# Kernel optimization log

Measured on AMD Instinct MI355X. Metric: run time of the kernel, lower is better.

## Reference

```python
import jax, jax.numpy as jnp
import numpy as np

H = 2048
V = 32000
B = 4            # 2 chosen + 2 rejected sequences
T = 1024
BETA = 0.1
IGNORE_INDEX = -100


def setup_inputs() -> dict:
    key = jax.random.key(0)
    k1, k2, k3, k4, k5 = jax.random.split(key, 5)
    x = jax.random.normal(k1, (B, T, H), dtype=jnp.float32)
    ref_x = jax.random.normal(k2, (B, T, H), dtype=jnp.float32)
    y = jax.random.randint(k3, (B, T), 0, V, dtype=jnp.int64)
    # Linear weights scaled ~1/sqrt(H) so logits are well-conditioned
    W = jax.random.normal(k4, (V, H), dtype=jnp.float32) * (1.0 / np.sqrt(H))
    W_ref = jax.random.normal(k5, (V, H), dtype=jnp.float32) * (1.0 / np.sqrt(H))
    return {"x": x, "ref_x": ref_x, "y": y, "W": W, "W_ref": W_ref}


def _avg_seq_logps(h, W, y, mask):
    # h: [B,T,H], W: [V,H] -> average per-sequence log-prob of the target tokens
    logits = jnp.einsum("bth,vh->btv", h, W)                 # [B,T,V]
    logps = jax.nn.log_softmax(logits, axis=-1)
    y_safe = jnp.where(mask, y, 0)
    per_tok = jnp.take_along_axis(logps, y_safe[..., None], axis=-1)[..., 0]  # [B,T]
    m = mask.astype(logps.dtype)
    return (per_tok * m).sum(-1) / m.sum(-1)                  # [B]


def reference(x, ref_x, y, W, W_ref):
    mask = y != IGNORE_INDEX
    logps = _avg_seq_logps(x, W, y, mask)
    # reference model path is computed without gradients (torch.no_grad in Liger)
    ref_logps = jax.lax.stop_gradient(_avg_seq_logps(ref_x, W_ref, y, mask))
    half = B // 2
    chosen, rejected = logps[:half], logps[half:]
    ref_chosen, ref_rejected = ref_logps[:half], ref_logps[half:]
    logits_diff = BETA * ((chosen - ref_chosen) - (rejected - ref_rejected))
    loss = -jax.nn.log_sigmoid(logits_diff).sum() / half
    return loss
```

## Files before the change

kernel.cpp:

```cpp
#include <hip/hip_runtime.h>
#include <cstdint>
#include <cstddef>

#define HDIM 2048
#define VOCAB 32000
#define BT 4096
#define NVB 125
#define BETA_F 0.1f
#define SCALE_X 16.0f
#define SCALE_W 64.0f
#define INV_SC (1.0f / (SCALE_X * SCALE_W))

typedef float f32x4 __attribute__((ext_vector_type(4)));
typedef long lx2 __attribute__((ext_vector_type(2)));

__device__ __forceinline__ void async_lds16(const void* g, void* l) {
  __builtin_amdgcn_global_load_lds(
      (__attribute__((address_space(1))) void*)g,
      (__attribute__((address_space(3))) void*)l,
      16, 0, 0);
}

#define BAR() __builtin_amdgcn_s_barrier()
#define LGKM0() do { asm volatile("s_waitcnt lgkmcnt(0)" ::: "memory"); \
                     __builtin_amdgcn_sched_barrier(0); } while (0)
#define VMCNT(n) do { asm volatile("s_waitcnt vmcnt(" #n ")" ::: "memory"); \
                      __builtin_amdgcn_sched_barrier(0); } while (0)

__global__ void cast_fp8_kernel(const float* __restrict__ src,
                                uint4* __restrict__ dst, int n16, float scale) {
  int i = blockIdx.x * blockDim.x + threadIdx.x;
  int stride = gridDim.x * blockDim.x;
  for (; i < n16; i += stride) {
    const float4* s = (const float4*)src + (size_t)i * 4;
    uint4 o;
    {
      float4 a = s[0];
      int r = __builtin_amdgcn_cvt_pk_fp8_f32(a.x * scale, a.y * scale, 0, false);
      o.x = __builtin_amdgcn_cvt_pk_fp8_f32(a.z * scale, a.w * scale, r, true);
    }
    {
      float4 a = s[1];
      int r = __builtin_amdgcn_cvt_pk_fp8_f32(a.x * scale, a.y * scale, 0, false);
      o.y = __builtin_amdgcn_cvt_pk_fp8_f32(a.z * scale, a.w * scale, r, true);
    }
    {
      float4 a = s[2];
      int r = __builtin_amdgcn_cvt_pk_fp8_f32(a.x * scale, a.y * scale, 0, false);
      o.z = __builtin_amdgcn_cvt_pk_fp8_f32(a.z * scale, a.w * scale, r, true);
    }
    {
      float4 a = s[3];
      int r = __builtin_amdgcn_cvt_pk_fp8_f32(a.x * scale, a.y * scale, 0, false);
      o.w = __builtin_amdgcn_cvt_pk_fp8_f32(a.z * scale, a.w * scale, r, true);
    }
    dst[i] = o;
  }
}

__global__ __launch_bounds__(512, 2) void gemm_lse256(
    const unsigned char* __restrict__ Xq,
    const unsigned char* __restrict__ Xrq,
    const unsigned char* __restrict__ Wq,
    const unsigned char* __restrict__ Wrq,
    float2* __restrict__ part) {
  __shared__ __align__(16) char lds[2][2][2][8192];

  const int tid = threadIdx.x;
  const int lane = tid & 63;
  const int w = tid >> 6;
  const int wm = w >> 2;
  const int wn = w & 3;
  const int which = blockIdx.y;

  const int lin = blockIdx.x;
  const int nl = (lin & 7) * 250 + (lin >> 3);
  const int mb = nl & 15;
  const int nb = nl >> 4;

  const unsigned char* A = which ? Xrq : Xq;
  const unsigned char* B = which ? Wrq : Wq;
  float2* pp = part + (size_t)which * BT * NVB;

  const int lanep = lane ^ ((lane & 32) >> 4);
  const int rw = w * 16 + (lanep >> 2);
  const int cw = (lanep & 3) * 16;
  const unsigned char* Ag = A + (size_t)(mb * 256 + rw) * HDIM + cw;
  const unsigned char* Bg = B + (size_t)(nb * 256 + rw) * HDIM + cw;

#define STAGE(opsel, buf, h, T) do {                                          \
    const unsigned char* _g = (opsel) ? Bg : Ag;                              \
    async_lds16(_g + (size_t)(h) * 128 * HDIM + (T) * 64,                     \
                &lds[buf][opsel][h][0] + w * 1024);                           \
  } while (0)

  const int l15 = lane & 15;
  const int kbyte = (lane >> 4) * 16;
#define FRAGP(d0, d1, halfptr, row) do {                                      \
    int _r = (row);                                                           \
    int _L = _r * 64 + kbyte;                                                 \
    lx2 _v = *(const lx2*)((halfptr) + (_L ^ (((_r >> 3) & 1) << 5)));        \
    d0 = _v.x; d1 = _v.y;                                                     \
  } while (0)

  const char* A0h = &lds[0][0][wm][0];
  const char* A1h = &lds[1][0][wm][0];
  const char* B0h = &lds[0][1][wn >> 1][0];
  const char* B1h = &lds[1][1][wn >> 1][0];
  const int brow = (wn & 1) * 64;

  f32x4 acc[8][4] = {};
  long aF[4][2], bF[4][2];

#define READ_A(base, mi0) do {                                                \
    _Pragma("unroll") for (int mi = 0; mi < 4; ++mi)                          \
      FRAGP(aF[mi][0], aF[mi][1], base, ((mi0) + mi) * 16 + l15);             \
  } while (0)
#define READ_B(base) do {                                                     \
    _Pragma("unroll") for (int ni = 0; ni < 4; ++ni)                          \
      FRAGP(bF[ni][0], bF[ni][1], base, brow + ni * 16 + l15);                \
  } while (0)
#define MFMA_Q(MI0, NI0) do {                                                 \
    __builtin_amdgcn_s_setprio(1);                                            \
    _Pragma("unroll") for (int kk = 0; kk < 2; ++kk)                          \
    _Pragma("unroll") for (int mi = 0; mi < 4; ++mi)                          \
    _Pragma("unroll") for (int ni = 0; ni < 2; ++ni)                          \
      acc[(MI0) + mi][(NI0) + ni] = __builtin_amdgcn_mfma_f32_16x16x32_fp8_fp8( \
          aF[mi][kk], bF[(NI0) + ni][kk], acc[(MI0) + mi][(NI0) + ni], 0, 0, 0); \
    __builtin_amdgcn_s_setprio(0);                                            \
  } while (0)

  STAGE(0, 0, 0, 0); STAGE(0, 0, 1, 0); STAGE(1, 0, 0, 0); STAGE(1, 0, 1, 0);
  STAGE(1, 1, 0, 1); STAGE(1, 1, 1, 1); STAGE(0, 1, 0, 1);
  VMCNT(3);
  BAR();

  for (int i = 0; i < 16; ++i) {
    const int t1 = 2 * i + 1;
    const int se = (2 * i + 2 > 30) ? 30 : 2 * i + 2;
    const int so = (2 * i + 3 > 31) ? 31 : 2 * i + 3;

    READ_A(A0h, 0);
    READ_B(B0h);
    STAGE(0, 1, 1, t1);
    BAR(); LGKM0();
    MFMA_Q(0, 0);
    BAR();

    STAGE(1, 0, 0, se);
    BAR(); LGKM0();
    MFMA_Q(0, 2);
    BAR();

    READ_A(A0h, 4);
    STAGE(1, 0, 1, se);
    BAR(); LGKM0();
    MFMA_Q(4, 0);
    BAR();

    STAGE(0, 0, 0, se);
    VMCNT(3);
    BAR();
    MFMA_Q(4, 2);
    BAR();

    READ_A(A1h, 0);
    READ_B(B1h);
    STAGE(0, 0, 1, se);
    BAR(); LGKM0();
    MFMA_Q(0, 0);
    BAR();

    STAGE(1, 1, 0, so);
    BAR(); LGKM0();
    MFMA_Q(0, 2);
    BAR();

    READ_A(A1h, 4);
    STAGE(1, 1, 1, so);
    BAR(); LGKM0();
    MFMA_Q(4, 0);
    BAR();

    STAGE(0, 1, 0, so);
    VMCNT(3);
    BAR();
    MFMA_Q(4, 2);
    BAR();
  }
  VMCNT(0);
  BAR();

  float* red = (float*)&lds[0][0][0][0];
#pragma unroll
  for (int mi = 0; mi < 8; ++mi) {
#pragma unroll
    for (int r = 0; r < 4; ++r) {
      float v0 = acc[mi][0][r] * INV_SC;
      float v1 = acc[mi][1][r] * INV_SC;
      float v2 = acc[mi][2][r] * INV_SC;
      float v3 = acc[mi][3][r] * INV_SC;
      float m = fmaxf(fmaxf(v0, v1), fmaxf(v2, v3));
#pragma unroll
      for (int o = 1; o < 16; o <<= 1) m = fmaxf(m, __shfl_xor(m, o, 64));
      float s = __expf(v0 - m) + __expf(v1 - m) + __expf(v2 - m) + __expf(v3 - m);
#pragma unroll
      for (int o = 1; o < 16; o <<= 1) s += __shfl_xor(s, o, 64);
      if (l15 == 0) {
        int row = wm * 128 + mi * 16 + (lane >> 4) * 4 + r;
        red[wn * 256 + row] = m;
        red[1024 + wn * 256 + row] = s;
      }
    }
  }
  __syncthreads();
  if (tid < 256) {
    float m0 = red[tid], m1 = red[256 + tid], m2 = red[512 + tid], m3 = red[768 + tid];
    float M = fmaxf(fmaxf(m0, m1), fmaxf(m2, m3));
    float S = red[1024 + tid] * __expf(m0 - M) + red[1280 + tid] * __expf(m1 - M) +
              red[1536 + tid] * __expf(m2 - M) + red[1792 + tid] * __expf(m3 - M);
    pp[(size_t)(mb * 256 + tid) * NVB + nb] = make_float2(M, S);
  }
#undef STAGE
#undef FRAGP
#undef READ_A
#undef READ_B
#undef MFMA_Q
}

__global__ void target_logit(const float* __restrict__ x, const float* __restrict__ xr,
                             const float* __restrict__ W, const float* __restrict__ Wr,
                             const int* __restrict__ y, float* __restrict__ tlog) {
  int wid = (blockIdx.x * blockDim.x + threadIdx.x) >> 6;
  int lane = threadIdx.x & 63;
  int which = wid >> 12;
  int tok = wid & 4095;
  int yy = y[tok];
  int ys = (yy == -100) ? 0 : yy;
  const float* xv = (which ? xr : x) + (size_t)tok * HDIM;
  const float* wv = (which ? Wr : W) + (size_t)ys * HDIM;
  const float4* x4 = (const float4*)xv;
  const float4* w4 = (const float4*)wv;
  float sum = 0.f;
  for (int i = lane; i < HDIM / 4; i += 64) {
    float4 a = x4[i], b = w4[i];
    sum += a.x * b.x + a.y * b.y + a.z * b.z + a.w * b.w;
  }
#pragma unroll
  for (int o = 1; o < 64; o <<= 1) sum += __shfl_xor(sum, o, 64);
  if (lane == 0) tlog[wid] = sum;
}

__global__ void lse_combine(const float2* __restrict__ part,
                            const float* __restrict__ tlog,
                            float* __restrict__ ptok) {
  int wid = (blockIdx.x * blockDim.x + threadIdx.x) >> 6;
  int lane = threadIdx.x & 63;
  const float2* p = part + (size_t)wid * NVB;
  float m = -INFINITY, s = 0.f;
  for (int i = lane; i < NVB; i += 64) {
    float2 v = p[i];
    float M = fmaxf(m, v.x);
    s = s * __expf(m - M) + v.y * __expf(v.x - M);
    m = M;
  }
#pragma unroll
  for (int o = 1; o < 64; o <<= 1) {
    float mo = __shfl_xor(m, o, 64);
    float so = __shfl_xor(s, o, 64);
    float M = fmaxf(m, mo);
    s = s * __expf(m - M) + so * __expf(mo - M);
    m = M;
  }
  if (lane == 0) ptok[wid] = tlog[wid] - (m + logf(s));
}

__global__ void final_loss(const float* __restrict__ ptok,
                           const int* __restrict__ y, float* __restrict__ out) {
  __shared__ float rs[256];
  __shared__ float rc[256];
  __shared__ float seq[8];
  int tid = threadIdx.x;
  for (int s = 0; s < 8; ++s) {
    int which = s >> 2, b = s & 3;
    float lsum = 0.f, lcnt = 0.f;
    for (int t = tid; t < 1024; t += 256) {
      int yy = y[b * 1024 + t];
      if (yy != -100) {
        lsum += ptok[which * 4096 + b * 1024 + t];
        lcnt += 1.f;
      }
    }
    rs[tid] = lsum; rc[tid] = lcnt;
    __syncthreads();
    for (int o = 128; o > 0; o >>= 1) {
      if (tid < o) { rs[tid] += rs[tid + o]; rc[tid] += rc[tid + o]; }
      __syncthreads();
    }
    if (tid == 0) seq[s] = rs[0] / rc[0];
    __syncthreads();
  }
  if (tid == 0) {
    float d0 = BETA_F * ((seq[0] - seq[4]) - (seq[2] - seq[6]));
    float d1 = BETA_F * ((seq[1] - seq[5]) - (seq[3] - seq[7]));
    auto sp = [](float a) { return fmaxf(a, 0.f) + log1pf(expf(-fabsf(a))); };
    out[0] = (sp(-d0) + sp(-d1)) * 0.5f;
  }
}

extern "C" void kernel_launch(void* const* d_in, const int* in_sizes, int n_in,
                              void* d_out, int out_size, void* d_ws, size_t ws_size,
                              hipStream_t stream) {
  const float* x   = (const float*)d_in[0];
  const float* xr  = (const float*)d_in[1];
  const int*   y   = (const int*)d_in[2];
  const float* Wf  = (const float*)d_in[3];
  const float* Wrf = (const float*)d_in[4];
  float* out = (float*)d_out;

  char* ws = (char*)d_ws;
  size_t off = 0;
  auto alloc = [&](size_t bytes) -> void* {
    void* p = ws + off;
    off = (off + bytes + 255) & ~(size_t)255;
    return p;
  };
  unsigned char* Xq  = (unsigned char*)alloc((size_t)BT * HDIM);
  unsigned char* Xrq = (unsigned char*)alloc((size_t)BT * HDIM);
  unsigned char* Wq  = (unsigned char*)alloc((size_t)VOCAB * HDIM);
  unsigned char* Wrq = (unsigned char*)alloc((size_t)VOCAB * HDIM);
  float2* part = (float2*)alloc((size_t)2 * BT * NVB * sizeof(float2));
  float*  tlog = (float*)alloc((size_t)2 * BT * sizeof(float));
  float*  ptok = (float*)alloc((size_t)2 * BT * sizeof(float));

  cast_fp8_kernel<<<2048, 256, 0, stream>>>(x,  (uint4*)Xq,  BT * HDIM / 16, SCALE_X);
  cast_fp8_kernel<<<2048, 256, 0, stream>>>(xr, (uint4*)Xrq, BT * HDIM / 16, SCALE_X);
  cast_fp8_kernel<<<2048, 256, 0, stream>>>(Wf,  (uint4*)Wq,  VOCAB * HDIM / 16, SCALE_W);
  cast_fp8_kernel<<<2048, 256, 0, stream>>>(Wrf, (uint4*)Wrq, VOCAB * HDIM / 16, SCALE_W);

  dim3 gg(2000, 2);
  gemm_lse256<<<gg, 512, 0, stream>>>(Xq, Xrq, Wq, Wrq, part);

  target_logit<<<2048, 256, 0, stream>>>(x, xr, Wf, Wrf, y, tlog);
  lse_combine<<<2048, 256, 0, stream>>>(part, tlog, ptok);
  final_loss<<<1, 256, 0, stream>>>(ptok, y, out);
}
```

Baseline: 986.5 us.

## Switch FP8 GEMM to 32x32x64 scaled MFMA with restructured staging pipeline

Replaces the 16x16x32 FP8 MFMA tiles with the gfx950 32x32x64 f8f6f4 scaled MFMA using identity scales, so each wave issues fewer, larger matrix instructions and reads wider 32-byte LDS fragments. The main loop goes from eight phases to four, with two async stages issued per phase and the vmcnt waits rearranged to match. The softmax epilogue is rewritten for the 32-row accumulator layout, reducing over 32 lanes instead of 16. The accumulator layout changes and the pipeline now has less interleaving, which could expose load latency or change register pressure.

```diff
diff --git a/kernel.cpp b/kernel.cpp
--- a/kernel.cpp
+++ b/kernel.cpp
@@ -10,9 +10,11 @@
 #define SCALE_X 16.0f
 #define SCALE_W 64.0f
 #define INV_SC (1.0f / (SCALE_X * SCALE_W))
-
-typedef float f32x4 __attribute__((ext_vector_type(4)));
-typedef long lx2 __attribute__((ext_vector_type(2)));
+#define ID_SCALE 0x7f7f7f7f
+
+typedef float f32x16 __attribute__((ext_vector_type(16)));
+typedef int i32x4v __attribute__((ext_vector_type(4)));
+typedef int i32x8v __attribute__((ext_vector_type(8)));
 
 __device__ __forceinline__ void async_lds16(const void* g, void* l) {
   __builtin_amdgcn_global_load_lds(
@@ -94,45 +96,48 @@
                 &lds[buf][opsel][h][0] + w * 1024);                           \
   } while (0)
 
-  const int l15 = lane & 15;
-  const int kbyte = (lane >> 4) * 16;
-#define FRAGP(d0, d1, halfptr, row) do {                                      \
+  const int l31 = lane & 31;
+  const int khalf = (lane >> 5) * 32;
+#define FRAG32(dst, halfptr, row) do {                                        \
     int _r = (row);                                                           \
-    int _L = _r * 64 + kbyte;                                                 \
-    lx2 _v = *(const lx2*)((halfptr) + (_L ^ (((_r >> 3) & 1) << 5)));        \
-    d0 = _v.x; d1 = _v.y;                                                     \
-  } while (0)
-
-  const char* A0h = &lds[0][0][wm][0];
-  const char* A1h = &lds[1][0][wm][0];
-  const char* B0h = &lds[0][1][wn >> 1][0];
-  const char* B1h = &lds[1][1][wn >> 1][0];
+    int _p = (_r * 64 + khalf) ^ (((_r >> 3) & 1) << 5);                      \
+    i32x4v _lo = *(const i32x4v*)((halfptr) + _p);                            \
+    i32x4v _hi = *(const i32x4v*)((halfptr) + _p + 16);                       \
+    dst = (i32x8v){_lo[0], _lo[1], _lo[2], _lo[3],                            \
+                   _hi[0], _hi[1], _hi[2], _hi[3]};                           \
+  } while (0)
+
+  const char* Ah[2] = { &lds[0][0][wm][0], &lds[1][0][wm][0] };
+  const char* Bh[2] = { &lds[0][1][wn >> 1][0], &lds[1][1][wn >> 1][0] };
   const int brow = (wn & 1) * 64;
 
-  f32x4 acc[8][4] = {};
-  long aF[4][2], bF[4][2];
-
-#define READ_A(base, mi0) do {                                                \
-    _Pragma("unroll") for (int mi = 0; mi < 4; ++mi)                          \
-      FRAGP(aF[mi][0], aF[mi][1], base, ((mi0) + mi) * 16 + l15);             \
-  } while (0)
-#define READ_B(base) do {                                                     \
-    _Pragma("unroll") for (int ni = 0; ni < 4; ++ni)                          \
-      FRAGP(bF[ni][0], bF[ni][1], base, brow + ni * 16 + l15);                \
-  } while (0)
-#define MFMA_Q(MI0, NI0) do {                                                 \
+  f32x16 acc[4][2] = {};
+  i32x8v aF0, aF1, bF0, bF1;
+
+#define READ_B(buf) do {                                                      \
+    FRAG32(bF0, Bh[buf], brow + l31);                                         \
+    FRAG32(bF1, Bh[buf], brow + 32 + l31);                                    \
+  } while (0)
+#define READ_A2(buf, mi0) do {                                                \
+    FRAG32(aF0, Ah[buf], (mi0) * 32 + l31);                                   \
+    FRAG32(aF1, Ah[buf], (mi0) * 32 + 32 + l31);                              \
+  } while (0)
+#define MFMA4(MI0) do {                                                       \
     __builtin_amdgcn_s_setprio(1);                                            \
-    _Pragma("unroll") for (int kk = 0; kk < 2; ++kk)                          \
-    _Pragma("unroll") for (int mi = 0; mi < 4; ++mi)                          \
-    _Pragma("unroll") for (int ni = 0; ni < 2; ++ni)                          \
-      acc[(MI0) + mi][(NI0) + ni] = __builtin_amdgcn_mfma_f32_16x16x32_fp8_fp8( \
-          aF[mi][kk], bF[(NI0) + ni][kk], acc[(MI0) + mi][(NI0) + ni], 0, 0, 0); \
+    acc[MI0][0] = __builtin_amdgcn_mfma_scale_f32_32x32x64_f8f6f4(            \
+        aF0, bF0, acc[MI0][0], 0, 0, 0, ID_SCALE, 0, ID_SCALE);               \
+    acc[MI0][1] = __builtin_amdgcn_mfma_scale_f32_32x32x64_f8f6f4(            \
+        aF0, bF1, acc[MI0][1], 0, 0, 0, ID_SCALE, 0, ID_SCALE);               \
+    acc[(MI0) + 1][0] = __builtin_amdgcn_mfma_scale_f32_32x32x64_f8f6f4(      \
+        aF1, bF0, acc[(MI0) + 1][0], 0, 0, 0, ID_SCALE, 0, ID_SCALE);         \
+    acc[(MI0) + 1][1] = __builtin_amdgcn_mfma_scale_f32_32x32x64_f8f6f4(      \
+        aF1, bF1, acc[(MI0) + 1][1], 0, 0, 0, ID_SCALE, 0, ID_SCALE);         \
     __builtin_amdgcn_s_setprio(0);                                            \
   } while (0)
 
   STAGE(0, 0, 0, 0); STAGE(0, 0, 1, 0); STAGE(1, 0, 0, 0); STAGE(1, 0, 1, 0);
-  STAGE(1, 1, 0, 1); STAGE(1, 1, 1, 1); STAGE(0, 1, 0, 1);
-  VMCNT(3);
+  STAGE(1, 1, 0, 1); STAGE(1, 1, 1, 1);
+  VMCNT(2);
   BAR();
 
   for (int i = 0; i < 16; ++i) {
@@ -140,52 +145,30 @@
     const int se = (2 * i + 2 > 30) ? 30 : 2 * i + 2;
     const int so = (2 * i + 3 > 31) ? 31 : 2 * i + 3;
 
-    READ_A(A0h, 0);
-    READ_B(B0h);
-    STAGE(0, 1, 1, t1);
+    READ_A2(0, 0); READ_B(0);
+    STAGE(0, 1, 0, t1); STAGE(0, 1, 1, t1);
     BAR(); LGKM0();
-    MFMA_Q(0, 0);
+    MFMA4(0);
     BAR();
 
-    STAGE(1, 0, 0, se);
+    READ_A2(0, 2);
+    STAGE(1, 0, 0, se); STAGE(1, 0, 1, se);
+    VMCNT(2);
     BAR(); LGKM0();
-    MFMA_Q(0, 2);
+    MFMA4(2);
     BAR();
 
-    READ_A(A0h, 4);
-    STAGE(1, 0, 1, se);
+    READ_A2(1, 0); READ_B(1);
+    STAGE(0, 0, 0, se); STAGE(0, 0, 1, se);
     BAR(); LGKM0();
-    MFMA_Q(4, 0);
+    MFMA4(0);
     BAR();
 
-    STAGE(0, 0, 0, se);
-    VMCNT(3);
-    BAR();
-    MFMA_Q(4, 2);
-    BAR();
-
-    READ_A(A1h, 0);
-    READ_B(B1h);
-    STAGE(0, 0, 1, se);
+    READ_A2(1, 2);
+    STAGE(1, 1, 0, so); STAGE(1, 1, 1, so);
+    VMCNT(2);
     BAR(); LGKM0();
-    MFMA_Q(0, 0);
-    BAR();
-
-    STAGE(1, 1, 0, so);
-    BAR(); LGKM0();
-    MFMA_Q(0, 2);
-    BAR();
-
-    READ_A(A1h, 4);
-    STAGE(1, 1, 1, so);
-    BAR(); LGKM0();
-    MFMA_Q(4, 0);
-    BAR();
-
-    STAGE(0, 1, 0, so);
-    VMCNT(3);
-    BAR();
-    MFMA_Q(4, 2);
+    MFMA4(2);
     BAR();
   }
   VMCNT(0);
@@ -193,21 +176,19 @@
 
   float* red = (float*)&lds[0][0][0][0];
 #pragma unroll
-  for (int mi = 0; mi < 8; ++mi) {
-#pragma unroll
-    for (int r = 0; r < 4; ++r) {
+  for (int mi = 0; mi < 4; ++mi) {
+#pragma unroll
+    for (int r = 0; r < 16; ++r) {
       float v0 = acc[mi][0][r] * INV_SC;
       float v1 = acc[mi][1][r] * INV_SC;
-      float v2 = acc[mi][2][r] * INV_SC;
-      float v3 = acc[mi][3][r] * INV_SC;
-      float m = fmaxf(fmaxf(v0, v1), fmaxf(v2, v3));
-#pragma unroll
-      for (int o = 1; o < 16; o <<= 1) m = fmaxf(m, __shfl_xor(m, o, 64));
-      float s = __expf(v0 - m) + __expf(v1 - m) + __expf(v2 - m) + __expf(v3 - m);
-#pragma unroll
-      for (int o = 1; o < 16; o <<= 1) s += __shfl_xor(s, o, 64);
-      if (l15 == 0) {
-        int row = wm * 128 + mi * 16 + (lane >> 4) * 4 + r;
+      float m = fmaxf(v0, v1);
+#pragma unroll
+      for (int o = 1; o < 32; o <<= 1) m = fmaxf(m, __shfl_xor(m, o, 64));
+      float s = __expf(v0 - m) + __expf(v1 - m);
+#pragma unroll
+      for (int o = 1; o < 32; o <<= 1) s += __shfl_xor(s, o, 64);
+      if (l31 == 0) {
+        int row = wm * 128 + mi * 32 + (r & 3) + 8 * (r >> 2) + 4 * (lane >> 5);
         red[wn * 256 + row] = m;
         red[1024 + wn * 256 + row] = s;
       }
@@ -222,10 +203,10 @@
     pp[(size_t)(mb * 256 + tid) * NVB + nb] = make_float2(M, S);
   }
 #undef STAGE
-#undef FRAGP
-#undef READ_A
+#undef FRAG32
 #undef READ_B
-#undef MFMA_Q
+#undef READ_A2
+#undef MFMA4
 }
 
 __global__ void target_logit(const float* __restrict__ x, const float* __restrict__ xr,
```

Result: slower. 1.031 ms (+4.5%).

## Restructure FP8 GEMM main loop with register-prefetched fragments and fewer barriers

Applied to the files above, without the earlier changes.

Rewrites the K-loop of the fused logits/logsumexp GEMM so each half-iteration issues all four global-to-LDS stages for a buffer at once. A and B fragments are split into lo/hi register sets so the next buffer's LDS reads overlap the current MFMA groups. The explicit lgkmcnt(0) waits and most of the per-quarter barriers are removed, leaving one vmcnt(0) plus barrier per buffer swap, with sched_barriers fixing instruction order. This aims to cut synchronisation stalls and raise MFMA issue density. In exchange, prefetch depth is shallower, and it relies on compiler-inserted LDS waits being correct against the async overwrites.

```diff
diff --git a/kernel.cpp b/kernel.cpp
--- a/kernel.cpp
+++ b/kernel.cpp
@@ -22,8 +22,7 @@
 }
 
 #define BAR() __builtin_amdgcn_s_barrier()
-#define LGKM0() do { asm volatile("s_waitcnt lgkmcnt(0)" ::: "memory"); \
-                     __builtin_amdgcn_sched_barrier(0); } while (0)
+#define SCHED0() __builtin_amdgcn_sched_barrier(0)
 #define VMCNT(n) do { asm volatile("s_waitcnt vmcnt(" #n ")" ::: "memory"); \
                       __builtin_amdgcn_sched_barrier(0); } while (0)
 
@@ -93,6 +92,10 @@
     async_lds16(_g + (size_t)(h) * 128 * HDIM + (T) * 64,                     \
                 &lds[buf][opsel][h][0] + w * 1024);                           \
   } while (0)
+#define STAGE4(buf, T) do {                                                   \
+    STAGE(0, buf, 0, T); STAGE(0, buf, 1, T);                                 \
+    STAGE(1, buf, 0, T); STAGE(1, buf, 1, T);                                 \
+  } while (0)
 
   const int l15 = lane & 15;
   const int kbyte = (lane >> 4) * 16;
@@ -103,93 +106,74 @@
     d0 = _v.x; d1 = _v.y;                                                     \
   } while (0)
 
-  const char* A0h = &lds[0][0][wm][0];
-  const char* A1h = &lds[1][0][wm][0];
-  const char* B0h = &lds[0][1][wn >> 1][0];
-  const char* B1h = &lds[1][1][wn >> 1][0];
+  const char* Ah[2] = { &lds[0][0][wm][0], &lds[1][0][wm][0] };
+  const char* Bh[2] = { &lds[0][1][wn >> 1][0], &lds[1][1][wn >> 1][0] };
   const int brow = (wn & 1) * 64;
 
   f32x4 acc[8][4] = {};
-  long aF[4][2], bF[4][2];
-
-#define READ_A(base, mi0) do {                                                \
+  long aLo[4][2], aHi[4][2], bLo[2][2], bHi[2][2];
+
+#define RD_ALO(buf) do {                                                      \
     _Pragma("unroll") for (int mi = 0; mi < 4; ++mi)                          \
-      FRAGP(aF[mi][0], aF[mi][1], base, ((mi0) + mi) * 16 + l15);             \
-  } while (0)
-#define READ_B(base) do {                                                     \
-    _Pragma("unroll") for (int ni = 0; ni < 4; ++ni)                          \
-      FRAGP(bF[ni][0], bF[ni][1], base, brow + ni * 16 + l15);                \
-  } while (0)
-#define MFMA_Q(MI0, NI0) do {                                                 \
+      FRAGP(aLo[mi][0], aLo[mi][1], Ah[buf], mi * 16 + l15);                  \
+  } while (0)
+#define RD_AHI(buf) do {                                                      \
+    _Pragma("unroll") for (int mi = 0; mi < 4; ++mi)                          \
+      FRAGP(aHi[mi][0], aHi[mi][1], Ah[buf], (4 + mi) * 16 + l15);            \
+  } while (0)
+#define RD_B01(buf) do {                                                      \
+    _Pragma("unroll") for (int ni = 0; ni < 2; ++ni)                          \
+      FRAGP(bLo[ni][0], bLo[ni][1], Bh[buf], brow + ni * 16 + l15);           \
+  } while (0)
+#define RD_B23(buf) do {                                                      \
+    _Pragma("unroll") for (int ni = 0; ni < 2; ++ni)                          \
+      FRAGP(bHi[ni][0], bHi[ni][1], Bh[buf], brow + (2 + ni) * 16 + l15);     \
+  } while (0)
+#define MFMA_Q(AG, BG, MI0, NI0) do {                                         \
     __builtin_amdgcn_s_setprio(1);                                            \
     _Pragma("unroll") for (int kk = 0; kk < 2; ++kk)                          \
     _Pragma("unroll") for (int mi = 0; mi < 4; ++mi)                          \
     _Pragma("unroll") for (int ni = 0; ni < 2; ++ni)                          \
       acc[(MI0) + mi][(NI0) + ni] = __builtin_amdgcn_mfma_f32_16x16x32_fp8_fp8( \
-          aF[mi][kk], bF[(NI0) + ni][kk], acc[(MI0) + mi][(NI0) + ni], 0, 0, 0); \
+          AG[mi][kk], BG[ni][kk], acc[(MI0) + mi][(NI0) + ni], 0, 0, 0);      \
     __builtin_amdgcn_s_setprio(0);                                            \
   } while (0)
 
-  STAGE(0, 0, 0, 0); STAGE(0, 0, 1, 0); STAGE(1, 0, 0, 0); STAGE(1, 0, 1, 0);
-  STAGE(1, 1, 0, 1); STAGE(1, 1, 1, 1); STAGE(0, 1, 0, 1);
-  VMCNT(3);
-  BAR();
+  STAGE4(0, 0);
+  STAGE4(1, 1);
+  VMCNT(4);
+  BAR(); SCHED0();
+  RD_ALO(0); RD_B01(0);
+  SCHED0();
 
   for (int i = 0; i < 16; ++i) {
-    const int t1 = 2 * i + 1;
     const int se = (2 * i + 2 > 30) ? 30 : 2 * i + 2;
     const int so = (2 * i + 3 > 31) ? 31 : 2 * i + 3;
 
-    READ_A(A0h, 0);
-    READ_B(B0h);
-    STAGE(0, 1, 1, t1);
-    BAR(); LGKM0();
-    MFMA_Q(0, 0);
-    BAR();
-
-    STAGE(1, 0, 0, se);
-    BAR(); LGKM0();
-    MFMA_Q(0, 2);
-    BAR();
-
-    READ_A(A0h, 4);
-    STAGE(1, 0, 1, se);
-    BAR(); LGKM0();
-    MFMA_Q(4, 0);
-    BAR();
-
-    STAGE(0, 0, 0, se);
-    VMCNT(3);
-    BAR();
-    MFMA_Q(4, 2);
-    BAR();
-
-    READ_A(A1h, 0);
-    READ_B(B1h);
-    STAGE(0, 0, 1, se);
-    BAR(); LGKM0();
-    MFMA_Q(0, 0);
-    BAR();
-
-    STAGE(1, 1, 0, so);
-    BAR(); LGKM0();
-    MFMA_Q(0, 2);
-    BAR();
-
-    READ_A(A1h, 4);
-    STAGE(1, 1, 1, so);
-    BAR(); LGKM0();
-    MFMA_Q(4, 0);
-    BAR();
-
-    STAGE(0, 1, 0, so);
-    VMCNT(3);
-    BAR();
-    MFMA_Q(4, 2);
-    BAR();
+    RD_B23(0); SCHED0();
+    MFMA_Q(aLo, bLo, 0, 0); SCHED0();
+    RD_AHI(0); SCHED0();
+    MFMA_Q(aLo, bHi, 0, 2); SCHED0();
+    MFMA_Q(aHi, bLo, 4, 0); SCHED0();
+    VMCNT(0);
+    BAR(); SCHED0();
+    STAGE4(0, se);
+    RD_ALO(1); RD_B01(1); SCHED0();
+    MFMA_Q(aHi, bHi, 4, 2); SCHED0();
+
+    RD_B23(1); SCHED0();
+    MFMA_Q(aLo, bLo, 0, 0); SCHED0();
+    RD_AHI(1); SCHED0();
+    MFMA_Q(aLo, bHi, 0, 2); SCHED0();
+    MFMA_Q(aHi, bLo, 4, 0); SCHED0();
+    VMCNT(0);
+    BAR(); SCHED0();
+    STAGE4(1, so);
+    RD_ALO(0); RD_B01(0); SCHED0();
+    MFMA_Q(aHi, bHi, 4, 2); SCHED0();
   }
   VMCNT(0);
-  BAR();
+  BAR(); SCHED0();
 
   float* red = (float*)&lds[0][0][0][0];
 #pragma unroll
@@ -222,9 +206,12 @@
     pp[(size_t)(mb * 256 + tid) * NVB + nb] = make_float2(M, S);
   }
 #undef STAGE
+#undef STAGE4
 #undef FRAGP
-#undef READ_A
-#undef READ_B
+#undef RD_ALO
+#undef RD_AHI
+#undef RD_B01
+#undef RD_B23
 #undef MFMA_Q
 }
 
```

Result: faster. 961.3 us (-2.5%).
